# Optimization experiments

Measured on AMD Instinct MI355X. Metric: run time of the kernel, lower is better.

Reference implementation:

```python
import jax, jax.numpy as jnp
import numpy as np

N, T, A, H, I, E = 50000, 25, 16, 128, 64, 800000
LN_EPS = 1e-5


def setup_inputs() -> dict:
    key = jax.random.key(0)
    ks = jax.random.split(key, 24)
    s = 0.05
    d = {}
    d['actions'] = jax.random.normal(ks[0], (N, T, A), jnp.float32)
    d['hidden'] = jax.random.normal(ks[1], (1, N, H), jnp.float32)
    d['src'] = jax.random.randint(ks[2], (E,), 0, N, jnp.int32)
    d['dst'] = jax.random.randint(ks[3], (E,), 0, N, jnp.int32)
    # GRU (torch layout: W_ih (3H, A), W_hh (3H, H), gates r,z,n)
    d['W_ih'] = jax.random.normal(ks[4], (3 * H, A), jnp.float32) * s
    d['W_hh'] = jax.random.normal(ks[5], (3 * H, H), jnp.float32) * s
    d['b_ih'] = jnp.zeros((3 * H,), jnp.float32)
    d['b_hh'] = jnp.zeros((3 * H,), jnp.float32)
    # LayerNorm feature_norm
    d['ln_g'] = jnp.ones((H,), jnp.float32)
    d['ln_b'] = jnp.zeros((H,), jnp.float32)
    # GraphConv (DGL norm='both'): weight (in, out), bias (out,)
    d['Wg'] = jax.random.normal(ks[6], (H, H), jnp.float32) * s
    d['bg'] = jnp.full((H,), 0.1, jnp.float32)
    # Four Gaussian heads (torch Linear: W (out, in))
    for i, name in enumerate(['zia_mu', 'zia_std', 'zig_mu', 'zig_std']):
        d['W_' + name] = jax.random.normal(ks[7 + i], (I, H), jnp.float32) * s
        d['b_' + name] = jnp.full((I,), 0.1, jnp.float32)
    return d


def _gru(x_tnf, h0, W_ih, W_hh, b_ih, b_hh):
    # x_tnf: (T, N, A); h0: (N, H). Precompute input projections for all steps.
    gi_all = jnp.einsum('tna,ga->tng', x_tnf, W_ih) + b_ih  # (T, N, 3H)

    def step(h, gi):
        gh = h @ W_hh.T + b_hh
        i_r, i_z, i_n = jnp.split(gi, 3, axis=-1)
        h_r, h_z, h_n = jnp.split(gh, 3, axis=-1)
        r = jax.nn.sigmoid(i_r + h_r)
        z = jax.nn.sigmoid(i_z + h_z)
        n = jnp.tanh(i_n + r * h_n)
        h_new = (1.0 - z) * n + z * h
        return h_new, None

    h_final, _ = jax.lax.scan(step, h0, gi_all)
    return h_final  # (N, H)


def _graph_conv(src, dst, x, Wg, bg):
    ones = jnp.ones((src.shape[0],), x.dtype)
    deg_out = jax.ops.segment_sum(ones, src, num_segments=N)
    deg_in = jax.ops.segment_sum(ones, dst, num_segments=N)
    norm_src = jnp.where(deg_out > 0, deg_out, 1.0) ** -0.5
    norm_dst = jnp.where(deg_in > 0, deg_in, 1.0) ** -0.5
    m = (x * norm_src[:, None])[src]                 # gather (E, H)
    agg = jax.ops.segment_sum(m, dst, num_segments=N)  # scatter-add (N, H)
    return (agg * norm_dst[:, None]) @ Wg + bg


def _layernorm(x, g, b):
    mu = jnp.mean(x, axis=-1, keepdims=True)
    var = jnp.var(x, axis=-1, keepdims=True)
    return (x - mu) * jax.lax.rsqrt(var + LN_EPS) * g + b


def reference(actions, hidden, src, dst, W_ih, W_hh, b_ih, b_hh, ln_g, ln_b,
              Wg, bg, W_zia_mu, b_zia_mu, W_zia_std, b_zia_std,
              W_zig_mu, b_zig_mu, W_zig_std, b_zig_std):
    x_tnf = jnp.transpose(actions, (1, 0, 2))  # actions.transpose(1,0)
    h = _gru(x_tnf, hidden[0], W_ih, W_hh, b_ih, b_hh)  # temp_rnn_state.squeeze(0)
    x = _layernorm(h, ln_g, ln_b)
    x = _graph_conv(src, dst, x, Wg, bg)
    zIA_mu = x @ W_zia_mu.T + b_zia_mu
    zIA_std = jax.nn.softplus(x @ W_zia_std.T + b_zia_std)
    zIG_mu = x @ W_zig_mu.T + b_zig_mu
    zIG_std = jax.nn.softplus(x @ W_zig_std.T + b_zig_std)
    # Normal(mu, std) params for both dists + rnn state
    return zIG_mu, zIG_std, zIA_mu, zIA_std, h
```

## Files before the change

kernel.cpp:

```cpp
#include <hip/hip_runtime.h>
#include <hip/hip_bf16.h>
#include <math.h>

constexpr int N_NODES = 50000;
constexpr int T_STEPS = 25;
constexpr int A_DIM   = 16;
constexpr int H_DIM   = 128;
constexpr int G3      = 3 * H_DIM;
constexpr int E_EDGES = 800000;
constexpr int I_DIM   = 64;
constexpr float LN_EPS = 1e-5f;
constexpr int NT = (N_NODES + 31) / 32;
constexpr int NT16 = N_NODES / 16;
constexpr int SXS = 408;
constexpr int SHS = 136;
constexpr int SCB = 196;

using bf16x8 = __attribute__((ext_vector_type(8))) short;
using f32x4  = __attribute__((ext_vector_type(4))) float;

static __device__ __forceinline__ float fast_rcp(float x) { return __builtin_amdgcn_rcpf(x); }
static __device__ __forceinline__ float sigm(float x) { return fast_rcp(1.f + __expf(-x)); }
static __device__ __forceinline__ float tanh_fast(float x) {
    return fmaf(2.f, fast_rcp(1.f + __expf(-2.f * x)), -1.f);
}
static __device__ __forceinline__ float softplus_f(float x) {
    return (x > 20.f) ? x : __logf(1.f + __expf(x));
}
static __device__ __forceinline__ unsigned short f2bf(float f) {
    __hip_bfloat16 b = __float2bfloat16(f);
    return *(unsigned short*)&b;
}
static __device__ __forceinline__ float2 bfp(unsigned int u) {
    union { unsigned int i; float f; } lo, hi;
    lo.i = u << 16; hi.i = u & 0xFFFF0000u;
    return make_float2(lo.f, hi.f);
}


__global__ void k_zero(int* deg_out, int* deg_in, int* cursor, int* esrc) {
    for (int i = blockIdx.x * blockDim.x + threadIdx.x; i < E_EDGES; i += gridDim.x * blockDim.x) {
        esrc[i] = 0;
        if (i < N_NODES) { deg_out[i] = 0; deg_in[i] = 0; cursor[i] = 0; }
    }
}

__global__ void k_hist(const int* __restrict__ src, const int* __restrict__ dst,
                       int* __restrict__ deg_out, int* __restrict__ deg_in) {
    for (int e = blockIdx.x * blockDim.x + threadIdx.x; e < E_EDGES; e += gridDim.x * blockDim.x) {
        int s = src[e], d = dst[e];
        if (s >= 0 && s < N_NODES) atomicAdd(&deg_out[s], 1);
        if (d >= 0 && d < N_NODES) atomicAdd(&deg_in[d], 1);
    }
}

__global__ void k_scan1(const int* __restrict__ deg, int* __restrict__ offs,
                        int* __restrict__ bsum) {
    __shared__ int wsum[4];
    const int tid = threadIdx.x, lane = tid & 63, wid = tid >> 6;
    const int i = blockIdx.x * 256 + tid;
    int v = (i < N_NODES) ? deg[i] : 0;
    int x = v;
    #pragma unroll
    for (int off = 1; off < 64; off <<= 1) {
        int yv = __shfl_up(x, off);
        if (lane >= off) x += yv;
    }
    if (lane == 63) wsum[wid] = x;
    __syncthreads();
    int pre = 0;
    #pragma unroll
    for (int w2 = 0; w2 < 3; ++w2) if (w2 < wid) pre += wsum[w2];
    if (i < N_NODES) offs[i] = pre + x - v;
    if (tid == 255) bsum[blockIdx.x] = pre + x;
}

__global__ void k_scan2(const int* __restrict__ bsum, int* __restrict__ boffs,
                        int* __restrict__ offs) {
    __shared__ int wsum[4];
    const int tid = threadIdx.x, lane = tid & 63, wid = tid >> 6;
    int v = (tid < SCB) ? bsum[tid] : 0;
    int x = v;
    #pragma unroll
    for (int off = 1; off < 64; off <<= 1) {
        int yv = __shfl_up(x, off);
        if (lane >= off) x += yv;
    }
    if (lane == 63) wsum[wid] = x;
    __syncthreads();
    int pre = 0;
    #pragma unroll
    for (int w2 = 0; w2 < 3; ++w2) if (w2 < wid) pre += wsum[w2];
    if (tid < SCB) boffs[tid] = pre + x - v;
    if (tid == 255) offs[N_NODES] = pre + x;
}

__global__ void k_scan3(const int* __restrict__ boffs, int* __restrict__ offs) {
    const int i = blockIdx.x * 256 + threadIdx.x;
    if (i < N_NODES) offs[i] += boffs[blockIdx.x];
}

__global__ void k_scatter(const int* __restrict__ src, const int* __restrict__ dst,
                          const int* __restrict__ offs, int* __restrict__ cursor,
                          int* __restrict__ esrc) {
    for (int e = blockIdx.x * blockDim.x + threadIdx.x; e < E_EDGES; e += gridDim.x * blockDim.x) {
        int d = dst[e];
        if (d < 0 || d >= N_NODES) continue;
        int pos = offs[d] + atomicAdd(&cursor[d], 1);
        if (pos >= 0 && pos < E_EDGES) esrc[pos] = src[e];
    }
}

__launch_bounds__(512, 4)
__global__ void k_gru(const float* __restrict__ actions,
                      const float* __restrict__ hidden,
                      const float* __restrict__ W_ih,
                      const float* __restrict__ W_hh,
                      const float* __restrict__ b_ih,
                      const float* __restrict__ b_hh,
                      const float* __restrict__ ln_g,
                      const float* __restrict__ ln_b,
                      const int* __restrict__ deg_out,
                      unsigned int* __restrict__ zA,
                      float* __restrict__ h_out) {
    __shared__ __align__(16) unsigned short sX[32 * SXS];
    __shared__ __align__(16) unsigned short sH[32 * SHS];

    const int tid  = threadIdx.x;
    const int w    = tid >> 6;
    const int lane = tid & 63;
    const int quad = lane >> 4;
    const int l16  = lane & 15;
    const int j    = 16 * w + l16;

    bf16x8 Bhh[3][4];
    #pragma unroll
    for (int gt = 0; gt < 3; ++gt) {
        const float* rowp = W_hh + (size_t)(gt * H_DIM + j) * H_DIM;
        #pragma unroll
        for (int kc = 0; kc < 4; ++kc) {
            const float* p = rowp + kc * 32 + quad * 8;
            float4 f0 = *(const float4*)p;
            float4 f1 = *(const float4*)(p + 4);
            bf16x8 v;
            v[0] = f2bf(f0.x); v[1] = f2bf(f0.y); v[2] = f2bf(f0.z); v[3] = f2bf(f0.w);
            v[4] = f2bf(f1.x); v[5] = f2bf(f1.y); v[6] = f2bf(f1.z); v[7] = f2bf(f1.w);
            Bhh[gt][kc] = v;
        }
    }
    bf16x8 Bih[3];
    #pragma unroll
    for (int gt = 0; gt < 3; ++gt) {
        bf16x8 v;
        #pragma unroll
        for (int q = 0; q < 8; ++q) v[q] = 0;
        if (quad < 2) {
            const float* p = W_ih + (size_t)(gt * H_DIM + j) * A_DIM + quad * 8;
            float4 f0 = *(const float4*)p;
            float4 f1 = *(const float4*)(p + 4);
            v[0] = f2bf(f0.x); v[1] = f2bf(f0.y); v[2] = f2bf(f0.z); v[3] = f2bf(f0.w);
            v[4] = f2bf(f1.x); v[5] = f2bf(f1.y); v[6] = f2bf(f1.z); v[7] = f2bf(f1.w);
        }
        Bih[gt] = v;
    }
    const float br   = b_ih[j] + b_hh[j];
    const float bz   = b_ih[H_DIM + j] + b_hh[H_DIM + j];
    const float bn_i = b_ih[2 * H_DIM + j];
    const float bn_h = b_hh[2 * H_DIM + j];
    const f32x4 cr0 = {br, br, br, br};
    const f32x4 cz0 = {bz, bz, bz, bz};
    const f32x4 cn0 = {bn_i, bn_i, bn_i, bn_i};
    const f32x4 ch0 = {bn_h, bn_h, bn_h, bn_h};
    const float2 lg2 = *(const float2*)&ln_g[2 * lane];
    const float2 lb2 = *(const float2*)&ln_b[2 * lane];

    for (int tile = blockIdx.x; tile < NT; tile += gridDim.x) {
        const int base = tile * 32;
        for (int idx = tid; idx < 32 * SXS; idx += 512) {
            int nl = idx / SXS, p = idx - nl * SXS;
            int n = base + nl;
            float f = (p < 400 && n < N_NODES) ? actions[(size_t)n * 400 + p] : 0.f;
            sX[nl * SXS + p] = f2bf(f);
        }
        for (int idx = tid; idx < 32 * H_DIM; idx += 512) {
            int nl = idx >> 7, k = idx & 127;
            int n = base + nl;
            sH[nl * SHS + k] = f2bf((n < N_NODES) ? hidden[(size_t)n * H_DIM + k] : 0.f);
        }
        float hp[2][4];
        #pragma unroll
        for (int m = 0; m < 2; ++m)
            #pragma unroll
            for (int r = 0; r < 4; ++r) {
                int n = base + m * 16 + quad * 4 + r;
                hp[m][r] = (n < N_NODES) ? hidden[(size_t)n * H_DIM + j] : 0.f;
            }
        __syncthreads();

        for (int t = 0; t < T_STEPS; ++t) {
            #pragma unroll
            for (int m = 0; m < 2; ++m) {
                bf16x8 ax = *(const bf16x8*)&sX[(m * 16 + l16) * SXS + t * 16 + quad * 8];
                if (quad >= 2) {
                    #pragma unroll
                    for (int q = 0; q < 8; ++q) ax[q] = 0;
                }
                f32x4 Cr = __builtin_amdgcn_mfma_f32_16x16x32_bf16(ax, Bih[0], cr0, 0, 0, 0);
                f32x4 Cz = __builtin_amdgcn_mfma_f32_16x16x32_bf16(ax, Bih[1], cz0, 0, 0, 0);
                f32x4 Cn = __builtin_amdgcn_mfma_f32_16x16x32_bf16(ax, Bih[2], cn0, 0, 0, 0);
                f32x4 Ch = ch0;
                #pragma unroll
                for (int kc = 0; kc < 4; ++kc) {
                    bf16x8 ah = *(const bf16x8*)&sH[(m * 16 + l16) * SHS + kc * 32 + quad * 8];
                    Cr = __builtin_amdgcn_mfma_f32_16x16x32_bf16(ah, Bhh[0][kc], Cr, 0, 0, 0);
                    Cz = __builtin_amdgcn_mfma_f32_16x16x32_bf16(ah, Bhh[1][kc], Cz, 0, 0, 0);
                    Ch = __builtin_amdgcn_mfma_f32_16x16x32_bf16(ah, Bhh[2][kc], Ch, 0, 0, 0);
                }
                #pragma unroll
                for (int r = 0; r < 4; ++r) {
                    float rg = sigm(Cr[r]);
                    float zg = sigm(Cz[r]);
                    float ng = tanh_fast(Cn[r] + rg * Ch[r]);
                    hp[m][r] = ng + zg * (hp[m][r] - ng);
                }
            }
            if (t < T_STEPS - 1) {
                __syncthreads();
                #pragma unroll
                for (int m = 0; m < 2; ++m)
                    #pragma unroll
                    for (int r = 0; r < 4; ++r)
                        sH[(m * 16 + quad * 4 + r) * SHS + j] = f2bf(hp[m][r]);
                __syncthreads();
            }
        }

        __syncthreads();
        float* sF = (float*)sX;
        #pragma unroll
        for (int m = 0; m < 2; ++m)
            #pragma unroll
            for (int r = 0; r < 4; ++r)
                sF[(m * 16 + quad * 4 + r) * 128 + j] = hp[m][r];
        __syncthreads();
        #pragma unroll
        for (int it = 0; it < 2; ++it) {
            int idx4 = tid + it * 512;
            int n = base + (idx4 >> 5);
            if (idx4 < 1024 && n < N_NODES)
                *(float4*)&h_out[(size_t)base * 128 + (size_t)idx4 * 4] =
                    *(const float4*)&sF[idx4 * 4];
        }
        if (zA) {
            #pragma unroll
            for (int i = 0; i < 4; ++i) {
                const int nl = w * 4 + i;
                const int n = base + nl;
                if (n < N_NODES) {
                    float v0 = sF[nl * 128 + 2 * lane];
                    float v1 = sF[nl * 128 + 2 * lane + 1];
                    float s = v0 + v1, qq = v0 * v0 + v1 * v1;
                    #pragma unroll
                    for (int mm = 32; mm; mm >>= 1) {
                        s  += __shfl_xor(s, mm);
                        qq += __shfl_xor(qq, mm);
                    }
                    float mu  = s * (1.f / H_DIM);
                    float var = fmaxf(qq * (1.f / H_DIM) - mu * mu, 0.f);
                    float inv = rsqrtf(var + LN_EPS);
                    int dg = deg_out[n];
                    float ns = rsqrtf((float)(dg > 0 ? dg : 1));
                    float z0 = (lg2.x * (v0 - mu) * inv + lb2.x) * ns;
                    float z1 = (lg2.y * (v1 - mu) * inv + lb2.y) * ns;
                    zA[(size_t)n * 64 + lane] =
                        ((unsigned int)f2bf(z1) << 16) | (unsigned int)f2bf(z0);
                }
            }
        }
        __syncthreads();
    }
}

__global__ void k_stats(const float* __restrict__ h, const int* __restrict__ deg_out,
                        float4* __restrict__ pqr) {
    int n = blockIdx.x * (blockDim.x >> 6) + (threadIdx.x >> 6);
    int lane = threadIdx.x & 63;
    if (n >= N_NODES) return;
    float v0 = h[(size_t)n * H_DIM + lane];
    float v1 = h[(size_t)n * H_DIM + 64 + lane];
    float s = v0 + v1, qq = v0 * v0 + v1 * v1;
    #pragma unroll
    for (int m = 32; m; m >>= 1) { s += __shfl_xor(s, m); qq += __shfl_xor(qq, m); }
    float mu = s * (1.f / H_DIM);
    float var = fmaxf(qq * (1.f / H_DIM) - mu * mu, 0.f);
    float inv = rsqrtf(var + LN_EPS);
    int d = deg_out[n];
    float ns = rsqrtf((float)(d > 0 ? d : 1));
    if (lane == 0) pqr[n] = make_float4(inv * ns, mu * inv * ns, ns, 0.f);
}

__global__ void k_comb(const float* __restrict__ Wg, const float* __restrict__ bg,
                       const float* __restrict__ Wig_mu, const float* __restrict__ big_mu,
                       const float* __restrict__ Wig_std, const float* __restrict__ big_std,
                       const float* __restrict__ Wia_mu, const float* __restrict__ bia_mu,
                       const float* __restrict__ Wia_std, const float* __restrict__ bia_std,
                       unsigned short* __restrict__ Wcomb, float* __restrict__ bcomb) {
    const int r = blockIdx.x;
    const int t = threadIdx.x;
    const int rr = r & 63;
    const float* Wh; const float* bh;
    switch (r >> 6) {
        case 0:  Wh = Wig_mu;  bh = big_mu;  break;
        case 1:  Wh = Wig_std; bh = big_std; break;
        case 2:  Wh = Wia_mu;  bh = bia_mu;  break;
        default: Wh = Wia_std; bh = bia_std; break;
    }
    __shared__ float sWr[H_DIM];
    sWr[t] = Wh[(size_t)rr * H_DIM + t];
    __syncthreads();
    const float4* wrow = (const float4*)(Wg + (size_t)t * H_DIM);
    float acc = 0.f;
    #pragma unroll 8
    for (int c4 = 0; c4 < 32; ++c4) {
        float4 v = wrow[c4];
        acc = fmaf(v.x, sWr[4 * c4    ], acc);
        acc = fmaf(v.y, sWr[4 * c4 + 1], acc);
        acc = fmaf(v.z, sWr[4 * c4 + 2], acc);
        acc = fmaf(v.w, sWr[4 * c4 + 3], acc);
    }
    Wcomb[r * H_DIM + t] = f2bf(acc);
    if (t == 0) {
        float s = bh[rr];
        for (int c = 0; c < H_DIM; ++c) s = fmaf(bg[c], sWr[c], s);
        bcomb[r] = s;
    }
}

template<bool USEZ>
__launch_bounds__(256)
__global__ void k_fused(const float* __restrict__ h,
                        const unsigned int* __restrict__ zA,
                        const int* __restrict__ offs, const int* __restrict__ esrc,
                        const float4* __restrict__ pqr,
                        const float* __restrict__ ln_g, const float* __restrict__ ln_b,
                        const unsigned short* __restrict__ Wcomb,
                        const float* __restrict__ bcomb,
                        float* __restrict__ out) {
    __shared__ __align__(16) unsigned short yl[16][136];

    const int tid  = threadIdx.x;
    const int w    = tid >> 6;
    const int lane = tid & 63;
    const int l16  = lane & 15;
    const int quad = lane >> 4;
    const long long NI = (long long)N_NODES * I_DIM;

    bf16x8 B[4][4];
    float bc[4];
    #pragma unroll
    for (int ct = 0; ct < 4; ++ct) {
        int col = (w * 4 + ct) * 16 + l16;
        bc[ct] = bcomb[col];
        #pragma unroll
        for (int kc = 0; kc < 4; ++kc)
            B[ct][kc] = *(const bf16x8*)&Wcomb[col * H_DIM + kc * 32 + quad * 8];
    }
    const float2 g2 = *(const float2*)&ln_g[2 * lane];
    const float2 b2 = *(const float2*)&ln_b[2 * lane];

    for (int tile = blockIdx.x; tile < NT16; tile += gridDim.x) {
        const int base = tile * 16;
        #pragma unroll
        for (int i = 0; i < 4; ++i) {
            const int nl = w * 4 + i;
            const int n  = base + nl;
            const int s0 = offs[n], s1 = offs[n + 1];
            float ax = 0.f, ay = 0.f, sq = 0.f, sr = 0.f;
            for (int e0 = s0; e0 < s1; e0 += 64) {
                int sv = (e0 + lane < s1) ? esrc[e0 + lane] : 0;
                const int cnt = min(64, s1 - e0);
                int k = 0;
                if (USEZ) {
                    for (; k + 4 <= cnt; k += 4) {
                        int sa = __shfl(sv, k),     sb = __shfl(sv, k + 1);
                        int sc = __shfl(sv, k + 2), sd = __shfl(sv, k + 3);
                        unsigned int za = zA[(size_t)sa * 64 + lane];
                        unsigned int zb = zA[(size_t)sb * 64 + lane];
                        unsigned int zc = zA[(size_t)sc * 64 + lane];
                        unsigned int zd = zA[(size_t)sd * 64 + lane];
                        float2 fa = bfp(za), fb = bfp(zb), fc = bfp(zc), fd = bfp(zd);
                        ax += (fa.x + fb.x) + (fc.x + fd.x);
                        ay += (fa.y + fb.y) + (fc.y + fd.y);
                    }
                    for (; k < cnt; ++k) {
                        int s = __shfl(sv, k);
                        float2 f = bfp(zA[(size_t)s * 64 + lane]);
                        ax += f.x; ay += f.y;
                    }
                } else {
                    for (; k + 2 <= cnt; k += 2) {
                        int sa = __shfl(sv, k), sb = __shfl(sv, k + 1);
                        float4 Pa = pqr[sa], Pb = pqr[sb];
                        float2 ha = *(const float2*)&h[(size_t)sa * H_DIM + 2 * lane];
                        float2 hb = *(const float2*)&h[(size_t)sb * H_DIM + 2 * lane];
                        ax = fmaf(Pa.x, ha.x, ax); ay = fmaf(Pa.x, ha.y, ay);
                        ax = fmaf(Pb.x, hb.x, ax); ay = fmaf(Pb.x, hb.y, ay);
                        sq += Pa.y + Pb.y; sr += Pa.z + Pb.z;
                    }
                    for (; k < cnt; ++k) {
                        int s = __shfl(sv, k);
                        float4 P = pqr[s];
                        float2 hv = *(const float2*)&h[(size_t)s * H_DIM + 2 * lane];
                        ax = fmaf(P.x, hv.x, ax); ay = fmaf(P.x, hv.y, ay);
                        sq += P.y; sr += P.z;
                    }
                }
            }
            const int d = s1 - s0;
            const float nd = rsqrtf((float)(d > 0 ? d : 1));
            float y0, y1;
            if (USEZ) { y0 = ax * nd; y1 = ay * nd; }
            else {
                y0 = (g2.x * (ax - sq) + b2.x * sr) * nd;
                y1 = (g2.y * (ay - sq) + b2.y * sr) * nd;
            }
            unsigned int pk = ((unsigned int)f2bf(y1) << 16) | (unsigned int)f2bf(y0);
            *(unsigned int*)&yl[nl][2 * lane] = pk;
        }
        __syncthreads();
        bf16x8 A[4];
        #pragma unroll
        for (int kc = 0; kc < 4; ++kc)
            A[kc] = *(const bf16x8*)&yl[l16][kc * 32 + quad * 8];
        #pragma unroll
        for (int ct = 0; ct < 4; ++ct) {
            f32x4 C = {0.f, 0.f, 0.f, 0.f};
            #pragma unroll
            for (int kc = 0; kc < 4; ++kc)
                C = __builtin_amdgcn_mfma_f32_16x16x32_bf16(A[kc], B[ct][kc], C, 0, 0, 0);
            const int col  = (w * 4 + ct) * 16 + l16;
            const int head = col >> 6;
            const int wi   = col & 63;
            const bool sp  = (col & 64) != 0;
            #pragma unroll
            for (int r_ = 0; r_ < 4; ++r_) {
                const int node = base + quad * 4 + r_;
                float v = C[r_] + bc[ct];
                if (sp) v = softplus_f(v);
                out[(long long)head * NI + (long long)node * I_DIM + wi] = v;
            }
        }
        __syncthreads();
    }
}

extern "C" void kernel_launch(void* const* d_in, const int* in_sizes, int n_in,
                              void* d_out, int out_size, void* d_ws, size_t ws_size,
                              hipStream_t stream) {
    const float* actions = (const float*)d_in[0];
    const float* hidden  = (const float*)d_in[1];
    const int*   src     = (const int*)d_in[2];
    const int*   dst     = (const int*)d_in[3];
    const float* W_ih    = (const float*)d_in[4];
    const float* W_hh    = (const float*)d_in[5];
    const float* b_ih    = (const float*)d_in[6];
    const float* b_hh    = (const float*)d_in[7];
    const float* ln_g    = (const float*)d_in[8];
    const float* ln_b    = (const float*)d_in[9];
    const float* Wg      = (const float*)d_in[10];
    const float* bg      = (const float*)d_in[11];
    const float* Wia_mu  = (const float*)d_in[12];
    const float* bia_mu  = (const float*)d_in[13];
    const float* Wia_std = (const float*)d_in[14];
    const float* bia_std = (const float*)d_in[15];
    const float* Wig_mu  = (const float*)d_in[16];
    const float* big_mu  = (const float*)d_in[17];
    const float* Wig_std = (const float*)d_in[18];
    const float* big_std = (const float*)d_in[19];
    float* out = (float*)d_out;

    char* w = (char*)d_ws;
    const size_t SZN = 200064;
    int*   deg_out = (int*)(w);
    int*   deg_in  = (int*)(w + SZN);
    int*   offs    = (int*)(w + 2 * SZN);
    int*   cursor  = (int*)(w + 2 * SZN + 200128);
    int*   esrc    = (int*)(w + 3 * SZN + 200128);
    char*  p2      = w + 3 * SZN + 200128 + 3200000;
    int*   bsum    = (int*)(p2);
    int*   boffs   = (int*)(p2 + 1024);
    unsigned short* Wcomb = (unsigned short*)(p2 + 2048);
    float* bcomb   = (float*)(p2 + 2048 + 65536);
    char*  p3      = p2 + 2048 + 65536 + 1024;
    float4* pqrA   = (float4*)p3;
    unsigned int* zA = (unsigned int*)p3;
    const bool useZ = ws_size >= (size_t)(4068928 + 12800000);

    k_zero<<<2048, 256, 0, stream>>>(deg_out, deg_in, cursor, esrc);
    k_hist<<<1024, 256, 0, stream>>>(src, dst, deg_out, deg_in);
    k_scan1<<<SCB, 256, 0, stream>>>(deg_in, offs, bsum);
    k_scan2<<<1, 256, 0, stream>>>(bsum, boffs, offs);
    k_scan3<<<SCB, 256, 0, stream>>>(boffs, offs);
    k_scatter<<<1024, 256, 0, stream>>>(src, dst, offs, cursor, esrc);
    k_comb<<<256, 128, 0, stream>>>(Wg, bg, Wig_mu, big_mu, Wig_std, big_std,
                                    Wia_mu, bia_mu, Wia_std, bia_std, Wcomb, bcomb);

    float* h_f = out + (size_t)4 * N_NODES * I_DIM;
    k_gru<<<NT, 512, 0, stream>>>(actions, hidden, W_ih, W_hh, b_ih, b_hh,
                                  ln_g, ln_b, deg_out, useZ ? zA : nullptr, h_f);

    if (useZ) {
        k_fused<true><<<NT16, 256, 0, stream>>>(h_f, zA, offs, esrc, pqrA,
                                                ln_g, ln_b, Wcomb, bcomb, out);
    } else {
        k_stats<<<(N_NODES + 3) / 4, 256, 0, stream>>>(h_f, deg_out, pqrA);
        k_fused<false><<<NT16, 256, 0, stream>>>(h_f, zA, offs, esrc, pqrA,
                                                 ln_g, ln_b, Wcomb, bcomb, out);
    }
}
```

Measured before the change: 637.4 us.

## Double-buffer GRU hidden state in LDS, deepen gather unroll, trim zero kernel

```diff
diff --git a/kernel.cpp b/kernel.cpp
--- a/kernel.cpp
+++ b/kernel.cpp
@@ -38,10 +38,9 @@
 }
 
 
-__global__ void k_zero(int* deg_out, int* deg_in, int* cursor, int* esrc) {
-    for (int i = blockIdx.x * blockDim.x + threadIdx.x; i < E_EDGES; i += gridDim.x * blockDim.x) {
-        esrc[i] = 0;
-        if (i < N_NODES) { deg_out[i] = 0; deg_in[i] = 0; cursor[i] = 0; }
+__global__ void k_zero(int* deg_out, int* deg_in, int* cursor) {
+    for (int i = blockIdx.x * blockDim.x + threadIdx.x; i < N_NODES; i += gridDim.x * blockDim.x) {
+        deg_out[i] = 0; deg_in[i] = 0; cursor[i] = 0;
     }
 }
 
@@ -124,7 +123,7 @@
                       unsigned int* __restrict__ zA,
                       float* __restrict__ h_out) {
     __shared__ __align__(16) unsigned short sX[32 * SXS];
-    __shared__ __align__(16) unsigned short sH[32 * SHS];
+    __shared__ __align__(16) unsigned short sH[2][32 * SHS];
 
     const int tid  = threadIdx.x;
     const int w    = tid >> 6;
@@ -185,7 +184,7 @@
         for (int idx = tid; idx < 32 * H_DIM; idx += 512) {
             int nl = idx >> 7, k = idx & 127;
             int n = base + nl;
-            sH[nl * SHS + k] = f2bf((n < N_NODES) ? hidden[(size_t)n * H_DIM + k] : 0.f);
+            sH[0][nl * SHS + k] = f2bf((n < N_NODES) ? hidden[(size_t)n * H_DIM + k] : 0.f);
         }
         float hp[2][4];
         #pragma unroll
@@ -197,7 +196,9 @@
             }
         __syncthreads();
 
+        int cur = 0;
         for (int t = 0; t < T_STEPS; ++t) {
+            const int nxt = cur ^ 1;
             #pragma unroll
             for (int m = 0; m < 2; ++m) {
                 bf16x8 ax = *(const bf16x8*)&sX[(m * 16 + l16) * SXS + t * 16 + quad * 8];
@@ -211,7 +212,7 @@
                 f32x4 Ch = ch0;
                 #pragma unroll
                 for (int kc = 0; kc < 4; ++kc) {
-                    bf16x8 ah = *(const bf16x8*)&sH[(m * 16 + l16) * SHS + kc * 32 + quad * 8];
+                    bf16x8 ah = *(const bf16x8*)&sH[cur][(m * 16 + l16) * SHS + kc * 32 + quad * 8];
                     Cr = __builtin_amdgcn_mfma_f32_16x16x32_bf16(ah, Bhh[0][kc], Cr, 0, 0, 0);
                     Cz = __builtin_amdgcn_mfma_f32_16x16x32_bf16(ah, Bhh[1][kc], Cz, 0, 0, 0);
                     Ch = __builtin_amdgcn_mfma_f32_16x16x32_bf16(ah, Bhh[2][kc], Ch, 0, 0, 0);
@@ -221,18 +222,14 @@
                     float rg = sigm(Cr[r]);
                     float zg = sigm(Cz[r]);
                     float ng = tanh_fast(Cn[r] + rg * Ch[r]);
-                    hp[m][r] = ng + zg * (hp[m][r] - ng);
+                    float h2 = ng + zg * (hp[m][r] - ng);
+                    hp[m][r] = h2;
+                    if (t < T_STEPS - 1)
+                        sH[nxt][(m * 16 + quad * 4 + r) * SHS + j] = f2bf(h2);
                 }
             }
-            if (t < T_STEPS - 1) {
-                __syncthreads();
-                #pragma unroll
-                for (int m = 0; m < 2; ++m)
-                    #pragma unroll
-                    for (int r = 0; r < 4; ++r)
-                        sH[(m * 16 + quad * 4 + r) * SHS + j] = f2bf(hp[m][r]);
-                __syncthreads();
-            }
+            cur = nxt;
+            if (t < T_STEPS - 1) __syncthreads();
         }
 
         __syncthreads();
@@ -381,6 +378,19 @@
                 const int cnt = min(64, s1 - e0);
                 int k = 0;
                 if (USEZ) {
+                    for (; k + 8 <= cnt; k += 8) {
+                        int s_[8];
+                        #pragma unroll
+                        for (int u = 0; u < 8; ++u) s_[u] = __shfl(sv, k + u);
+                        unsigned int z_[8];
+                        #pragma unroll
+                        for (int u = 0; u < 8; ++u) z_[u] = zA[(size_t)s_[u] * 64 + lane];
+                        #pragma unroll
+                        for (int u = 0; u < 8; ++u) {
+                            float2 f = bfp(z_[u]);
+                            ax += f.x; ay += f.y;
+                        }
+                    }
                     for (; k + 4 <= cnt; k += 4) {
                         int sa = __shfl(sv, k),     sb = __shfl(sv, k + 1);
                         int sc = __shfl(sv, k + 2), sd = __shfl(sv, k + 3);
@@ -496,7 +506,7 @@
     unsigned int* zA = (unsigned int*)p3;
     const bool useZ = ws_size >= (size_t)(4068928 + 12800000);
 
-    k_zero<<<2048, 256, 0, stream>>>(deg_out, deg_in, cursor, esrc);
+    k_zero<<<256, 256, 0, stream>>>(deg_out, deg_in, cursor);
     k_hist<<<1024, 256, 0, stream>>>(src, dst, deg_out, deg_in);
     k_scan1<<<SCB, 256, 0, stream>>>(deg_in, offs, bsum);
     k_scan2<<<1, 256, 0, stream>>>(bsum, boffs, offs);
```

New measurement: 629.8 us. About the same (-1.2%).
